# Optimization experiments

Measured on AMD Instinct MI355X. Metric: run time of the kernel, lower is better.

## Reference

```python
import jax, jax.numpy as jnp
import numpy as np

EPS = 1e-8  # torch F.cosine_similarity default eps


def setup_inputs() -> dict:
    key = jax.random.key(0)
    k1, k2 = jax.random.split(key)
    proto = jax.random.normal(k1, (1, 10, 640, 1, 196), dtype=jnp.float32)
    query = jax.random.normal(k2, (1, 300, 640, 1, 196), dtype=jnp.float32)
    return {"proto": proto, "query": query}


def reference(proto, query):
    # squeeze episode and singleton spatial dims: [way, C, N], [Q, C, N]
    p = proto[0, :, :, 0, :]
    q = query[0, :, :, 0, :]
    # cosine similarity over C between every proto spatial location i and
    # query spatial location j -> sim[q, w, i, j]
    # dots via a single contraction instead of the repeated/broadcast tensors
    dots = jnp.einsum('wci,qcj->qwij', p, q)               # [Q, way, N, N]
    p_norm = jnp.sqrt(jnp.sum(p * p, axis=1))              # [way, N]
    q_norm = jnp.sqrt(jnp.sum(q * q, axis=1))              # [Q, N]
    denom = p_norm[None, :, :, None] * q_norm[:, None, None, :]
    sim = dots / jnp.maximum(denom, EPS)
    return sim
```

## Files before the change

kernel.cpp:

```cpp
#include <hip/hip_runtime.h>
#include <stdint.h>

#define QN    300
#define WN    10
#define CD    640
#define IJ    196
#define MROWS 1960
#define NTOT  58800
#define OUTQ  384160
#define EPSV  1e-8f

#define BM    256
#define BN    256
#define BK    64
#define BUFE  ((BM + BN) * BK)
#define NTK   (CD / BK)

#define MT_TILES 8
#define NT_TILES 230
#define NWG      (MT_TILES * NT_TILES)
#define CPX      (NWG / 8)

typedef __attribute__((ext_vector_type(8))) short bf16x8;
typedef __attribute__((ext_vector_type(4))) float f32x4;

__device__ __forceinline__ unsigned short f2bf(float f) {
    uint32_t u = __float_as_uint(f);
    u += 0x7FFFu + ((u >> 16) & 1u);
    return (unsigned short)(u >> 16);
}

__device__ __forceinline__ void gload16(const void* g, void* l) {
    __builtin_amdgcn_global_load_lds(
        (const __attribute__((address_space(1))) void*)g,
        (__attribute__((address_space(3))) void*)l,
        16, 0, 0);
}

__global__ __launch_bounds__(256)
void prep_kernel(const float* __restrict__ X, uint4* __restrict__ XT,
                 float* __restrict__ nrm)
{
    __shared__ float T[128][21];
    __shared__ float ssL[16][17];

    const int b  = blockIdx.y;
    const int i0 = blockIdx.x * 16;
    const int t  = threadIdx.x;
    const float* Xb = X + (size_t)b * (CD * IJ);

    const int cA  = t >> 2;
    const int i4  = (t & 3) * 4;
    const int iv  = i0 + i4;
    const bool liv = (iv <= IJ - 4);

    const int il = t >> 4;
    const int u  = t & 15;
    float ss = 0.f;

    const int ig   = i0 + il;
    const bool wok = (ig < IJ);
    const int rowg = b * IJ + (wok ? ig : IJ - 1);
    const int uxor = rowg & 7;

    for (int cc = 0; cc < CD / 128; ++cc) {
        #pragma unroll
        for (int pass = 0; pass < 2; ++pass) {
            int cl = pass * 64 + cA;
            int c  = cc * 128 + cl;
            float4 v = make_float4(0.f, 0.f, 0.f, 0.f);
            if (liv) v = *(const float4*)&Xb[(size_t)c * IJ + iv];
            T[cl][i4 + 0] = v.x; T[cl][i4 + 1] = v.y;
            T[cl][i4 + 2] = v.z; T[cl][i4 + 3] = v.w;
        }
        __syncthreads();
        float v[8];
        #pragma unroll
        for (int r = 0; r < 8; ++r) { v[r] = T[u * 8 + r][il]; ss += v[r] * v[r]; }
        if (wok) {
            union { unsigned short s[8]; uint4 q; } pk;
            #pragma unroll
            for (int r = 0; r < 8; ++r) pk.s[r] = f2bf(v[r]);
            int us = (u & 8) | ((u & 7) ^ uxor);
            XT[(size_t)rowg * (CD / 8) + cc * 16 + us] = pk.q;
        }
        __syncthreads();
    }

    ssL[il][u] = ss;
    __syncthreads();
    if (t < 16) {
        int igw = i0 + t;
        if (igw < IJ) {
            float s = 0.f;
            #pragma unroll
            for (int k = 0; k < 16; ++k) s += ssL[t][k];
            nrm[b * IJ + igw] = sqrtf(s);
        }
    }
}

__global__ __launch_bounds__(512, 2)
void gemm_kernel(const uint4* __restrict__ AT, const uint4* __restrict__ BT,
                 const float* __restrict__ pn, const float* __restrict__ qn,
                 float* __restrict__ out)
{
    __shared__ unsigned short lds[2 * BUFE];

    const int bid = blockIdx.x;
    const int swz = (bid & 7) * CPX + (bid >> 3);
    const int mt  = swz & (MT_TILES - 1);
    const int nt  = swz >> 3;
    const int m0  = mt * BM;
    const int n0  = nt * BN;

    const int t  = threadIdx.x;
    const int w  = t >> 6, l = t & 63;
    const int fr = l & 15, fq = l >> 4;
    const int wm0 = (w >> 2) * 128;
    const int wn0 = (w & 3) * 64;

    const int lr = l >> 3, lu = l & 7;
    int ra00 = m0 +   0 + w * 8 + lr; if (ra00 > MROWS - 1) ra00 = MROWS - 1;
    int ra01 = m0 +  64 + w * 8 + lr; if (ra01 > MROWS - 1) ra01 = MROWS - 1;
    int ra10 = m0 + 128 + w * 8 + lr; if (ra10 > MROWS - 1) ra10 = MROWS - 1;
    int ra11 = m0 + 192 + w * 8 + lr; if (ra11 > MROWS - 1) ra11 = MROWS - 1;
    int rb00 = n0 +   0 + w * 8 + lr; if (rb00 > NTOT - 1) rb00 = NTOT - 1;
    int rb01 = n0 +  64 + w * 8 + lr; if (rb01 > NTOT - 1) rb01 = NTOT - 1;
    int rb10 = n0 + 128 + w * 8 + lr; if (rb10 > NTOT - 1) rb10 = NTOT - 1;
    int rb11 = n0 + 192 + w * 8 + lr; if (rb11 > NTOT - 1) rb11 = NTOT - 1;
    const uint4* ga00 = AT + (size_t)ra00 * 80 + lu;
    const uint4* ga01 = AT + (size_t)ra01 * 80 + lu;
    const uint4* ga10 = AT + (size_t)ra10 * 80 + lu;
    const uint4* ga11 = AT + (size_t)ra11 * 80 + lu;
    const uint4* gb00 = BT + (size_t)rb00 * 80 + lu;
    const uint4* gb01 = BT + (size_t)rb01 * 80 + lu;
    const uint4* gb10 = BT + (size_t)rb10 * 80 + lu;
    const uint4* gb11 = BT + (size_t)rb11 * 80 + lu;
    const int la00 = (  0 + w * 8) * 64;
    const int la01 = ( 64 + w * 8) * 64;
    const int la10 = (128 + w * 8) * 64;
    const int la11 = (192 + w * 8) * 64;
    const int lb00 = BM * 64 + (  0 + w * 8) * 64;
    const int lb01 = BM * 64 + ( 64 + w * 8) * 64;
    const int lb10 = BM * 64 + (128 + w * 8) * 64;
    const int lb11 = BM * 64 + (192 + w * 8) * 64;

    const int fqS0 = fq << 3;
    const int fqS1 = (fq + 4) << 3;
    int baA[8], kyA[8], baB[4], kyB[4];
    #pragma unroll
    for (int i = 0; i < 8; ++i) {
        int rowa = wm0 + i * 16 + fr;
        baA[i] = rowa * 64;  kyA[i] = (rowa & 7) << 3;
    }
    #pragma unroll
    for (int i = 0; i < 4; ++i) {
        int rowb = wn0 + i * 16 + fr;
        baB[i] = BM * 64 + rowb * 64;  kyB[i] = (rowb & 7) << 3;
    }

    f32x4 acc[8][4];
    #pragma unroll
    for (int a = 0; a < 8; ++a)
        #pragma unroll
        for (int bb = 0; bb < 4; ++bb)
            acc[a][bb] = (f32x4){0.f, 0.f, 0.f, 0.f};

#define STAGE_A(OFF)                                                      \
    gload16(ga00, (char*)&lds[(OFF) + la00]); ga00 += 8;                  \
    gload16(ga01, (char*)&lds[(OFF) + la01]); ga01 += 8;                  \
    gload16(ga10, (char*)&lds[(OFF) + la10]); ga10 += 8;                  \
    gload16(ga11, (char*)&lds[(OFF) + la11]); ga11 += 8;
#define STAGE_B0(OFF)                                                     \
    gload16(gb00, (char*)&lds[(OFF) + lb00]); gb00 += 8;                  \
    gload16(gb01, (char*)&lds[(OFF) + lb01]); gb01 += 8;
#define STAGE_B1(OFF)                                                     \
    gload16(gb10, (char*)&lds[(OFF) + lb10]); gb10 += 8;                  \
    gload16(gb11, (char*)&lds[(OFF) + lb11]); gb11 += 8;

#define BARRIER  __builtin_amdgcn_s_barrier()
#define LGKM0    do { asm volatile("s_waitcnt lgkmcnt(0)" ::: "memory");  \
                      __builtin_amdgcn_sched_barrier(0); } while (0)
#define VMCNT0   asm volatile("s_waitcnt vmcnt(0)" ::: "memory")

#define MFMA_Q(MB, BF)                                                    \
    _Pragma("unroll")                                                     \
    for (int mm = 0; mm < 4; ++mm)                                        \
        _Pragma("unroll")                                                 \
        for (int nn = 0; nn < 4; ++nn)                                    \
            acc[(MB) + mm][nn] = __builtin_amdgcn_mfma_f32_16x16x32_bf16( \
                af[mm], BF[nn], acc[(MB) + mm][nn], 0, 0, 0);

#define TILE(STG)                                                         \
  { bf16x8 af[4], bf0[4], bf1[4];                                         \
                      \
    _Pragma("unroll")                                                     \
    for (int mm = 0; mm < 4; ++mm)                                        \
        af[mm] = *(const bf16x8*)&lds[oc + baA[mm] + (fqS0 ^ kyA[mm])];   \
    _Pragma("unroll")                                                     \
    for (int nn = 0; nn < 4; ++nn)                                        \
        bf0[nn] = *(const bf16x8*)&lds[oc + baB[nn] + (fqS0 ^ kyB[nn])];  \
    if (STG) { STAGE_A(os); }                                             \
    BARRIER; LGKM0;                                                       \
    __builtin_amdgcn_s_setprio(1); MFMA_Q(0, bf0);                        \
    __builtin_amdgcn_s_setprio(0); BARRIER;                               \
                       \
    _Pragma("unroll")                                                     \
    for (int mm = 0; mm < 4; ++mm)                                        \
        af[mm] = *(const bf16x8*)&lds[oc + baA[4+mm] + (fqS0 ^ kyA[4+mm])];\
    if (STG) { STAGE_B0(os); }                                            \
    BARRIER; LGKM0;                                                       \
    __builtin_amdgcn_s_setprio(1); MFMA_Q(4, bf0);                        \
    __builtin_amdgcn_s_setprio(0); BARRIER;                               \
                       \
    _Pragma("unroll")                                                     \
    for (int mm = 0; mm < 4; ++mm)                                        \
        af[mm] = *(const bf16x8*)&lds[oc + baA[mm] + (fqS1 ^ kyA[mm])];   \
    _Pragma("unroll")                                                     \
    for (int nn = 0; nn < 4; ++nn)                                        \
        bf1[nn] = *(const bf16x8*)&lds[oc + baB[nn] + (fqS1 ^ kyB[nn])];  \
    if (STG) { STAGE_B1(os); }                                            \
    BARRIER; LGKM0;                                                       \
    __builtin_amdgcn_s_setprio(1); MFMA_Q(0, bf1);                        \
    __builtin_amdgcn_s_setprio(0); BARRIER;                               \
           \
    _Pragma("unroll")                                                     \
    for (int mm = 0; mm < 4; ++mm)                                        \
        af[mm] = *(const bf16x8*)&lds[oc + baA[4+mm] + (fqS1 ^ kyA[4+mm])];\
    BARRIER; LGKM0;                                                       \
    __builtin_amdgcn_s_setprio(1); MFMA_Q(4, bf1);                        \
    __builtin_amdgcn_s_setprio(0);                                        \
    VMCNT0; BARRIER;                                                      \
    int tswp = oc; oc = os; os = tswp;                                    \
  }

    STAGE_A(0); STAGE_B0(0); STAGE_B1(0);
    VMCNT0;
    BARRIER;

    int oc = 0, os = BUFE;
    for (int tt = 0; tt < NTK - 1; ++tt) {
        TILE(1)
    }
    TILE(0)

#undef TILE
#undef MFMA_Q
#undef STAGE_A
#undef STAGE_B0
#undef STAGE_B1

    float  rqv[4];
    int    nvalid[4];
    size_t obase[4];
    #pragma unroll
    for (int tn = 0; tn < 4; ++tn) {
        int n = n0 + wn0 + tn * 16 + fr;
        nvalid[tn] = (n < NTOT);
        int nc = nvalid[tn] ? n : NTOT - 1;
        int q  = nc / IJ;
        int j  = nc - q * IJ;
        rqv[tn]   = qn[nc];
        obase[tn] = (size_t)q * OUTQ + j;
    }
    #pragma unroll
    for (int tm = 0; tm < 8; ++tm) {
        #pragma unroll
        for (int rr = 0; rr < 4; ++rr) {
            int m = m0 + wm0 + tm * 16 + fq * 4 + rr;
            if (m < MROWS) {
                float rp = pn[m];
                #pragma unroll
                for (int tn = 0; tn < 4; ++tn) {
                    if (nvalid[tn]) {
                        float d = fmaxf(rp * rqv[tn], EPSV);
                        out[obase[tn] + (size_t)m * IJ] =
                            acc[tm][tn][rr] * __builtin_amdgcn_rcpf(d);
                    }
                }
            }
        }
    }
}

#define BMF 128
#define BNF 224
#define LPAD 40
__global__ __launch_bounds__(512, 4)
void sim_fallback(const float* __restrict__ proto,
                  const float* __restrict__ query,
                  float* __restrict__ out)
{
    __shared__ unsigned short As[BMF][LPAD];
    __shared__ unsigned short Bs[BNF][LPAD];
    __shared__ float redA[4][BMF];
    __shared__ float redB[2][BNF];
    __shared__ float rpS[BMF];
    __shared__ float rqS[BNF];

    const int tid = threadIdx.x;
    const int m0  = blockIdx.x * BMF;
    const int q   = blockIdx.y;

    const int mA  = tid & (BMF - 1);
    const int krA = tid >> 7;
    const int wiA = m0 + mA;
    const bool va = (wiA < MROWS);
    const int wA  = va ? (wiA / IJ) : 0;
    const int iA  = va ? (wiA - wA * IJ) : 0;
    const float* pA = proto + wA * (CD * IJ) + iA;

    const bool tb  = (tid < 448);
    const int jB   = tb ? (tid % BNF) : 0;
    const int krB  = tb ? (tid / BNF) : 0;
    const bool vb  = tb && (jB < IJ);
    const float* qB = query + q * (CD * IJ) + jB;

    float ssA = 0.f, ssB = 0.f;

    const int wv   = tid >> 6;
    const int lane = tid & 63;
    const int wm0  = (wv >> 1) * 32;
    const int wn0  = (wv & 1) * 112;
    const int fr   = lane & 15;
    const int fq   = lane >> 4;

    f32x4 acc[2][7];
    #pragma unroll
    for (int a = 0; a < 2; a++)
        #pragma unroll
        for (int b = 0; b < 7; b++)
            acc[a][b] = (f32x4){0.f, 0.f, 0.f, 0.f};

    for (int it = 0; it < CD / 32; ++it) {
        const int c0 = it * 32;
        {
            float v[8];
            #pragma unroll
            for (int e = 0; e < 8; e++) {
                int c = c0 + krA * 8 + e;
                v[e] = va ? pA[c * IJ] : 0.f;
            }
            #pragma unroll
            for (int e = 0; e < 8; e++) ssA += v[e] * v[e];
            union { unsigned short s[8]; uint4 u; } pk;
            #pragma unroll
            for (int e = 0; e < 8; e++) pk.s[e] = f2bf(v[e]);
            *(uint4*)&As[mA][krA * 8] = pk.u;
        }
        if (tb) {
            #pragma unroll
            for (int h = 0; h < 2; ++h) {
                float v[8];
                #pragma unroll
                for (int e = 0; e < 8; e++) {
                    int c = c0 + krB * 16 + h * 8 + e;
                    v[e] = vb ? qB[c * IJ] : 0.f;
                }
                #pragma unroll
                for (int e = 0; e < 8; e++) ssB += v[e] * v[e];
                union { unsigned short s[8]; uint4 u; } pk;
                #pragma unroll
                for (int e = 0; e < 8; e++) pk.s[e] = f2bf(v[e]);
                *(uint4*)&Bs[jB][krB * 16 + h * 8] = pk.u;
            }
        }
        __syncthreads();
        bf16x8 af[2], bfv[7];
        #pragma unroll
        for (int tm = 0; tm < 2; tm++)
            af[tm] = *(const bf16x8*)&As[wm0 + tm * 16 + fr][fq * 8];
        #pragma unroll
        for (int tn = 0; tn < 7; tn++)
            bfv[tn] = *(const bf16x8*)&Bs[wn0 + tn * 16 + fr][fq * 8];
        #pragma unroll
        for (int tm = 0; tm < 2; tm++)
            #pragma unroll
            for (int tn = 0; tn < 7; tn++)
                acc[tm][tn] = __builtin_amdgcn_mfma_f32_16x16x32_bf16(
                    af[tm], bfv[tn], acc[tm][tn], 0, 0, 0);
        __syncthreads();
    }

    redA[krA][mA] = ssA;
    if (tb) redB[krB][jB] = ssB;
    __syncthreads();
    if (tid < BMF) {
        rpS[tid] = sqrtf(redA[0][tid] + redA[1][tid] + redA[2][tid] + redA[3][tid]);
    } else if (tid >= 256 && tid < 256 + BNF) {
        int j = tid - 256;
        rqS[j] = sqrtf(redB[0][j] + redB[1][j]);
    }
    __syncthreads();

    #pragma unroll
    for (int tm = 0; tm < 2; tm++) {
        #pragma unroll
        for (int tn = 0; tn < 7; tn++) {
            #pragma unroll
            for (int r = 0; r < 4; r++) {
                int rl = wm0 + tm * 16 + fq * 4 + r;
                int cl = wn0 + tn * 16 + fr;
                int wi = m0 + rl;
                if (wi < MROWS && cl < IJ) {
                    float denom = fmaxf(rpS[rl] * rqS[cl], 1e-8f);
                    out[(size_t)(q * MROWS + wi) * IJ + cl] = acc[tm][tn][r] / denom;
                }
            }
        }
    }
}

extern "C" void kernel_launch(void* const* d_in, const int* in_sizes, int n_in,
                              void* d_out, int out_size, void* d_ws, size_t ws_size,
                              hipStream_t stream) {
    const float* proto = (const float*)d_in[0];
    const float* query = (const float*)d_in[1];
    float* out = (float*)d_out;

    const size_t off_pT = 0;
    const size_t off_qT = 2508800;
    const size_t off_pn = 77772800;
    const size_t off_qn = 77780736;
    const size_t need   = 78015936;

    if (ws_size < need) {
        dim3 grid((MROWS + BMF - 1) / BMF, QN);
        sim_fallback<<<grid, 512, 0, stream>>>(proto, query, out);
        return;
    }

    char* ws = (char*)d_ws;
    uint4* pT = (uint4*)(ws + off_pT);
    uint4* qT = (uint4*)(ws + off_qT);
    float* pn = (float*)(ws + off_pn);
    float* qn = (float*)(ws + off_qn);

    prep_kernel<<<dim3(13, QN), 256, 0, stream>>>(query, qT, qn);
    prep_kernel<<<dim3(13, WN), 256, 0, stream>>>(proto, pT, pn);

    gemm_kernel<<<dim3(NWG), 512, 0, stream>>>(pT, qT, pn, qn, out);
}
```

Measured before the change: 393.3 us.

## Restructure GEMM main loop into finer-grained staggered load and MFMA pipeline

Rewrites the K-loop of the bf16 MFMA GEMM so that global-to-LDS loads are issued in half-tile pieces interleaved with four compute phases, two K tiles per iteration. It waits with partial `vmcnt` instead of draining all loads at each tile end, and regroups the LDS fragment reads so each phase loads both k-halves for a 4x2 block of MFMAs. The goal is to keep the next tile's memory traffic in flight while the math runs and to cut stalls at barriers. In exchange, the prologue and loop tail issue loads past the last K tile, reading extra global memory into unused buffers, and the barrier and waitcnt ordering is harder to verify.

```diff
diff --git a/kernel.cpp b/kernel.cpp
--- a/kernel.cpp
+++ b/kernel.cpp
@@ -167,89 +167,103 @@
         for (int bb = 0; bb < 4; ++bb)
             acc[a][bb] = (f32x4){0.f, 0.f, 0.f, 0.f};
 
-#define STAGE_A(OFF)                                                      \
-    gload16(ga00, (char*)&lds[(OFF) + la00]); ga00 += 8;                  \
-    gload16(ga01, (char*)&lds[(OFF) + la01]); ga01 += 8;                  \
-    gload16(ga10, (char*)&lds[(OFF) + la10]); ga10 += 8;                  \
-    gload16(ga11, (char*)&lds[(OFF) + la11]); ga11 += 8;
-#define STAGE_B0(OFF)                                                     \
-    gload16(gb00, (char*)&lds[(OFF) + lb00]); gb00 += 8;                  \
-    gload16(gb01, (char*)&lds[(OFF) + lb01]); gb01 += 8;
-#define STAGE_B1(OFF)                                                     \
-    gload16(gb10, (char*)&lds[(OFF) + lb10]); gb10 += 8;                  \
-    gload16(gb11, (char*)&lds[(OFF) + lb11]); gb11 += 8;
-
-#define BARRIER  __builtin_amdgcn_s_barrier()
-#define LGKM0    do { asm volatile("s_waitcnt lgkmcnt(0)" ::: "memory");  \
-                      __builtin_amdgcn_sched_barrier(0); } while (0)
-#define VMCNT0   asm volatile("s_waitcnt vmcnt(0)" ::: "memory")
-
-#define MFMA_Q(MB, BF)                                                    \
+#define ST2(PA, PB, LA, LB)                                               \
+    gload16(PA, (char*)&lds[(LA)]); PA += 8;                              \
+    gload16(PB, (char*)&lds[(LB)]); PB += 8;
+
+#define RD_A(OC, G)                                                       \
     _Pragma("unroll")                                                     \
-    for (int mm = 0; mm < 4; ++mm)                                        \
+    for (int mm = 0; mm < 4; ++mm) {                                      \
+        af[mm]   = *(const bf16x8*)&lds[(OC) + baA[(G)+mm]                \
+                                        + (fqS0 ^ kyA[(G)+mm])];          \
+        af[4+mm] = *(const bf16x8*)&lds[(OC) + baA[(G)+mm]                \
+                                        + (fqS1 ^ kyA[(G)+mm])];          \
+    }
+#define RD_B(BV, OC, G)                                                   \
+    _Pragma("unroll")                                                     \
+    for (int nn = 0; nn < 2; ++nn) {                                      \
+        BV[nn]   = *(const bf16x8*)&lds[(OC) + baB[(G)+nn]                \
+                                        + (fqS0 ^ kyB[(G)+nn])];          \
+        BV[2+nn] = *(const bf16x8*)&lds[(OC) + baB[(G)+nn]                \
+                                        + (fqS1 ^ kyB[(G)+nn])];          \
+    }
+#define MF(MB, NB, BV)                                                    \
+    _Pragma("unroll")                                                     \
+    for (int ks = 0; ks < 2; ++ks)                                        \
         _Pragma("unroll")                                                 \
-        for (int nn = 0; nn < 4; ++nn)                                    \
-            acc[(MB) + mm][nn] = __builtin_amdgcn_mfma_f32_16x16x32_bf16( \
-                af[mm], BF[nn], acc[(MB) + mm][nn], 0, 0, 0);
-
-#define TILE(STG)                                                         \
-  { bf16x8 af[4], bf0[4], bf1[4];                                         \
-                      \
-    _Pragma("unroll")                                                     \
-    for (int mm = 0; mm < 4; ++mm)                                        \
-        af[mm] = *(const bf16x8*)&lds[oc + baA[mm] + (fqS0 ^ kyA[mm])];   \
-    _Pragma("unroll")                                                     \
-    for (int nn = 0; nn < 4; ++nn)                                        \
-        bf0[nn] = *(const bf16x8*)&lds[oc + baB[nn] + (fqS0 ^ kyB[nn])];  \
-    if (STG) { STAGE_A(os); }                                             \
-    BARRIER; LGKM0;                                                       \
-    __builtin_amdgcn_s_setprio(1); MFMA_Q(0, bf0);                        \
-    __builtin_amdgcn_s_setprio(0); BARRIER;                               \
-                       \
-    _Pragma("unroll")                                                     \
-    for (int mm = 0; mm < 4; ++mm)                                        \
-        af[mm] = *(const bf16x8*)&lds[oc + baA[4+mm] + (fqS0 ^ kyA[4+mm])];\
-    if (STG) { STAGE_B0(os); }                                            \
-    BARRIER; LGKM0;                                                       \
-    __builtin_amdgcn_s_setprio(1); MFMA_Q(4, bf0);                        \
-    __builtin_amdgcn_s_setprio(0); BARRIER;                               \
-                       \
-    _Pragma("unroll")                                                     \
-    for (int mm = 0; mm < 4; ++mm)                                        \
-        af[mm] = *(const bf16x8*)&lds[oc + baA[mm] + (fqS1 ^ kyA[mm])];   \
-    _Pragma("unroll")                                                     \
-    for (int nn = 0; nn < 4; ++nn)                                        \
-        bf1[nn] = *(const bf16x8*)&lds[oc + baB[nn] + (fqS1 ^ kyB[nn])];  \
-    if (STG) { STAGE_B1(os); }                                            \
-    BARRIER; LGKM0;                                                       \
-    __builtin_amdgcn_s_setprio(1); MFMA_Q(0, bf1);                        \
-    __builtin_amdgcn_s_setprio(0); BARRIER;                               \
-           \
-    _Pragma("unroll")                                                     \
-    for (int mm = 0; mm < 4; ++mm)                                        \
-        af[mm] = *(const bf16x8*)&lds[oc + baA[4+mm] + (fqS1 ^ kyA[4+mm])];\
-    BARRIER; LGKM0;                                                       \
-    __builtin_amdgcn_s_setprio(1); MFMA_Q(4, bf1);                        \
-    __builtin_amdgcn_s_setprio(0);                                        \
-    VMCNT0; BARRIER;                                                      \
-    int tswp = oc; oc = os; os = tswp;                                    \
-  }
-
-    STAGE_A(0); STAGE_B0(0); STAGE_B1(0);
-    VMCNT0;
-    BARRIER;
-
-    int oc = 0, os = BUFE;
-    for (int tt = 0; tt < NTK - 1; ++tt) {
-        TILE(1)
-    }
-    TILE(0)
-
-#undef TILE
-#undef MFMA_Q
-#undef STAGE_A
-#undef STAGE_B0
-#undef STAGE_B1
+        for (int mm = 0; mm < 4; ++mm)                                    \
+            _Pragma("unroll")                                             \
+            for (int nn = 0; nn < 2; ++nn)                                \
+                acc[(MB)+mm][(NB)+nn] =                                   \
+                    __builtin_amdgcn_mfma_f32_16x16x32_bf16(              \
+                        af[ks*4+mm], BV[ks*2+nn],                         \
+                        acc[(MB)+mm][(NB)+nn], 0, 0, 0);
+
+#define BAR    __builtin_amdgcn_s_barrier()
+#define LGKM0  do { asm volatile("s_waitcnt lgkmcnt(0)" ::: "memory");    \
+                    __builtin_amdgcn_sched_barrier(0); } while (0)
+#define VMC(N) asm volatile("s_waitcnt vmcnt(" #N ")" ::: "memory")
+#define PRIO1  __builtin_amdgcn_s_setprio(1)
+#define PRIO0  __builtin_amdgcn_s_setprio(0)
+
+    ST2(ga00, ga01, la00, la01);
+    ST2(gb00, gb01, lb00, lb01);
+    ST2(ga10, ga11, la10, la11);
+    ST2(gb10, gb11, lb10, lb11);
+    ST2(ga00, ga01, BUFE + la00, BUFE + la01);
+    VMC(2); BAR;
+
+    for (int i5 = 0; i5 < NTK / 2; ++i5) {
+        bf16x8 af[8], b0[4], b1[4];
+        RD_A(0, 0); RD_B(b0, 0, 0);
+        ST2(gb00, gb01, BUFE + lb00, BUFE + lb01);
+        BAR; LGKM0;
+        PRIO1; MF(0, 0, b0); PRIO0;
+        BAR;
+        RD_B(b1, 0, 2);
+        ST2(ga10, ga11, BUFE + la10, BUFE + la11);
+        BAR; LGKM0;
+        PRIO1; MF(0, 2, b1); PRIO0;
+        BAR;
+        RD_A(0, 4);
+        ST2(gb10, gb11, BUFE + lb10, BUFE + lb11);
+        BAR; LGKM0;
+        PRIO1; MF(4, 2, b1); PRIO0;
+        BAR;
+        ST2(ga00, ga01, la00, la01);
+        PRIO1; MF(4, 0, b0); PRIO0;
+        VMC(2); BAR;
+        RD_A(BUFE, 0); RD_B(b0, BUFE, 0);
+        ST2(gb00, gb01, lb00, lb01);
+        BAR; LGKM0;
+        PRIO1; MF(0, 0, b0); PRIO0;
+        BAR;
+        RD_B(b1, BUFE, 2);
+        ST2(ga10, ga11, la10, la11);
+        BAR; LGKM0;
+        PRIO1; MF(0, 2, b1); PRIO0;
+        BAR;
+        RD_A(BUFE, 4);
+        ST2(gb10, gb11, lb10, lb11);
+        BAR; LGKM0;
+        PRIO1; MF(4, 2, b1); PRIO0;
+        BAR;
+        ST2(ga00, ga01, BUFE + la00, BUFE + la01);
+        PRIO1; MF(4, 0, b0); PRIO0;
+        VMC(2); BAR;
+    }
+
+    VMC(0);
+
+#undef ST2
+#undef RD_A
+#undef RD_B
+#undef MF
+#undef BAR
+#undef LGKM0
+#undef VMC
+#undef PRIO1
+#undef PRIO0
 
     float  rqv[4];
     int    nvalid[4];
```

Measured after the change: 393.0 us. Within noise of the previous version (-0.1%).
